# Optimization experiments

Hardware: AMD Instinct MI355X
Metric: run time of the kernel (lower is better)

Reference implementation:

```python
import jax, jax.numpy as jnp
import numpy as np

D = 256          # d_model
NH = 8           # n_heads
HD = D // NH
LEV = 3          # n_levels
NP = 4           # n_points
DFF = 1024       # d_ffn
B = 8            # batch
LQ = 3600        # 60*60 queries (hardcoded in get_reference_points)
SHAPES = np.array([[60, 60], [30, 30], [15, 15]], dtype=np.int64)
LIN = int((SHAPES[:, 0] * SHAPES[:, 1]).sum())  # 4725
START = np.concatenate([[0], np.cumsum(SHAPES[:, 0] * SHAPES[:, 1])[:-1]]).astype(np.int64)


def setup_inputs() -> dict:
    key = jax.random.key(0)
    ks = iter(jax.random.split(key, 32))
    def lin(k, o, i):
        return jax.random.normal(k, (o, i), jnp.float32) * 0.02
    return {
        "tgt": jax.random.normal(next(ks), (LQ, B, D), jnp.float32),
        "query_pos": jax.random.normal(next(ks), (1, 1, D), jnp.float32),
        "src": jax.random.normal(next(ks), (B, LIN, D), jnp.float32),
        "src_spatial_shapes": jnp.asarray(SHAPES),
        "level_start_index": jnp.asarray(START),
        "in_proj_w": lin(next(ks), 3 * D, D),
        "in_proj_b": jnp.zeros((3 * D,), jnp.float32),
        "out_proj_w": lin(next(ks), D, D),
        "out_proj_b": jnp.zeros((D,), jnp.float32),
        "samp_off_w": lin(next(ks), NH * LEV * NP * 2, D),
        "samp_off_b": jax.random.normal(next(ks), (NH * LEV * NP * 2,), jnp.float32) * 0.5,
        "attn_w_w": lin(next(ks), NH * LEV * NP, D),
        "attn_w_b": jnp.zeros((NH * LEV * NP,), jnp.float32),
        "value_proj_w": lin(next(ks), D, D),
        "value_proj_b": jnp.zeros((D,), jnp.float32),
        "cross_out_w": lin(next(ks), D, D),
        "cross_out_b": jnp.zeros((D,), jnp.float32),
        "ln1_g": jnp.ones((D,), jnp.float32), "ln1_b": jnp.zeros((D,), jnp.float32),
        "ln2_g": jnp.ones((D,), jnp.float32), "ln2_b": jnp.zeros((D,), jnp.float32),
        "ln3_g": jnp.ones((D,), jnp.float32), "ln3_b": jnp.zeros((D,), jnp.float32),
        "ffn_w1": lin(next(ks), DFF, D), "ffn_b1": jnp.zeros((DFF,), jnp.float32),
        "ffn_w2": lin(next(ks), D, DFF), "ffn_b2": jnp.zeros((D,), jnp.float32),
    }


def _ln(x, g, b, eps=1e-5):
    m = x.mean(-1, keepdims=True)
    v = ((x - m) ** 2).mean(-1, keepdims=True)
    return (x - m) * jax.lax.rsqrt(v + eps) * g + b


def _self_attn(q_in, k_in, v_in, wqkv, bqkv, wo, bo):
    # torch nn.MultiheadAttention semantics, inputs laid out (seq, batch, embed)
    S, N, _ = q_in.shape
    q = (q_in @ wqkv[:D].T + bqkv[:D]).reshape(S, N, NH, HD)
    k = (k_in @ wqkv[D:2 * D].T + bqkv[D:2 * D]).reshape(S, N, NH, HD)
    v = (v_in @ wqkv[2 * D:].T + bqkv[2 * D:]).reshape(S, N, NH, HD)
    logits = jnp.einsum('snhd,tnhd->nhst', q, k) / np.sqrt(HD).astype(np.float32)
    a = jax.nn.softmax(logits, -1)
    ctx = jnp.einsum('nhst,tnhd->snhd', a, v).reshape(S, N, D)
    return ctx @ wo.T + bo


def _bilinear(v_l, loc, Hl, Wl):
    # v_l: [B, NH, Hl*Wl, HD]; loc: [B, NH, LQ, NP, 2] normalized in [0,1]
    # grid_sample(align_corners=False, padding=zeros): pixel = loc*size - 0.5
    x = loc[..., 0] * Wl - 0.5
    y = loc[..., 1] * Hl - 0.5
    x0 = jnp.floor(x); y0 = jnp.floor(y)
    fx = x - x0; fy = y - y0
    x0 = x0.astype(jnp.int32); y0 = y0.astype(jnp.int32)
    def corner(yi, xi, w):
        valid = ((xi >= 0) & (xi < Wl) & (yi >= 0) & (yi < Hl)).astype(v_l.dtype)
        idx = jnp.clip(yi, 0, Hl - 1) * Wl + jnp.clip(xi, 0, Wl - 1)
        b, h, lq, p = idx.shape
        g = jnp.take_along_axis(v_l, idx.reshape(b, h, lq * p)[..., None], axis=2)
        return g.reshape(b, h, lq, p, HD) * (w * valid)[..., None]
    return (corner(y0, x0, (1 - fx) * (1 - fy))
            + corner(y0, x0 + 1, fx * (1 - fy))
            + corner(y0 + 1, x0, (1 - fx) * fy)
            + corner(y0 + 1, x0 + 1, fx * fy))


def _msdeform(query, ref, src, wso, bso, waw, baw, wv, bv, wo, bo):
    Bq, Lq, _ = query.shape
    value = (src @ wv.T + bv).reshape(Bq, LIN, NH, HD).transpose(0, 2, 1, 3)  # [B,NH,LIN,HD]
    off = (query @ wso.T + bso).reshape(Bq, Lq, NH, LEV, NP, 2)
    aw = (query @ waw.T + baw).reshape(Bq, Lq, NH, LEV * NP)
    aw = jax.nn.softmax(aw, -1).reshape(Bq, Lq, NH, LEV, NP)
    normalizer = jnp.asarray(SHAPES[:, ::-1].copy(), jnp.float32)  # (W, H) per level
    loc = ref[:, :, None, :, None, :] + off / normalizer[None, None, None, :, None, :]
    out = jnp.zeros((Bq, NH, Lq, HD), query.dtype)
    for l in range(LEV):
        Hl, Wl = int(SHAPES[l, 0]), int(SHAPES[l, 1])
        s = int(START[l])
        v_l = value[:, :, s:s + Hl * Wl]
        loc_l = loc[:, :, :, l].transpose(0, 2, 1, 3, 4)      # [B,NH,LQ,NP,2]
        sampled = _bilinear(v_l, loc_l, Hl, Wl)               # [B,NH,LQ,NP,HD]
        out = out + (sampled * aw[:, :, :, l].transpose(0, 2, 1, 3)[..., None]).sum(3)
    out = out.transpose(0, 2, 1, 3).reshape(Bq, Lq, D)
    return out @ wo.T + bo


def _reference_points():
    Hh = Ww = 60
    ys = (jnp.arange(Hh, dtype=jnp.float32) + 0.5) / Hh
    xs = (jnp.arange(Ww, dtype=jnp.float32) + 0.5) / Ww
    yy, xx = jnp.meshgrid(ys, xs, indexing='ij')
    ref = jnp.stack([xx.reshape(-1), yy.reshape(-1)], -1)[None]  # [1, 3600, 2]
    return jnp.broadcast_to(ref[:, :, None, :], (1, Hh * Ww, LEV, 2))


def reference(tgt, query_pos, src, src_spatial_shapes, level_start_index,
              in_proj_w, in_proj_b, out_proj_w, out_proj_b,
              samp_off_w, samp_off_b, attn_w_w, attn_w_b,
              value_proj_w, value_proj_b, cross_out_w, cross_out_b,
              ln1_g, ln1_b, ln2_g, ln2_b, ln3_g, ln3_b,
              ffn_w1, ffn_b1, ffn_w2, ffn_b2):
    # dropout layers are identity (eval mode). spatial shapes are static metadata
    # (SHAPES/START) since slicing sizes must be static under jit.
    q = (tgt + query_pos).transpose(1, 0, 2)
    tgt2 = _self_attn(q, q, tgt.transpose(1, 0, 2), in_proj_w, in_proj_b, out_proj_w, out_proj_b)
    t = _ln(tgt + tgt2.transpose(1, 0, 2), ln2_g, ln2_b)
    ref = _reference_points()
    tq = t.transpose(1, 0, 2)  # permute(1,0,2) -> [B, LQ, D]
    tgt2 = _msdeform(tq + query_pos, ref, src, samp_off_w, samp_off_b,
                     attn_w_w, attn_w_b, value_proj_w, value_proj_b,
                     cross_out_w, cross_out_b)
    tq = _ln(tq + tgt2, ln1_g, ln1_b)
    ff = jax.nn.relu(tq @ ffn_w1.T + ffn_b1) @ ffn_w2.T + ffn_b2
    tq = _ln(tq + ff, ln3_g, ln3_b)
    return tq.transpose(1, 0, 2)  # [LQ, B, D]
```

## Files before the change

kernel.cpp:

```cpp
#include <hip/hip_runtime.h>
#include <hip/hip_bf16.h>
#include <cstddef>
#include <cstdint>

#define D_MODEL 256
#define NHEAD   8
#define HDIM    32
#define NLEV    3
#define NPNT    4
#define DFF     1024
#define BATCH   8
#define LQ      3600
#define LIN     4725
#define MROWS   (BATCH*LQ)

typedef short bf16x8 __attribute__((ext_vector_type(8)));
typedef float f32x4  __attribute__((ext_vector_type(4)));

__device__ __forceinline__ unsigned short f2b(float x) {
    unsigned int u = __float_as_uint(x);
    unsigned int r = (u + 0x7fffu + ((u >> 16) & 1u)) >> 16;
    return (unsigned short)r;
}
__device__ __forceinline__ float b2f(unsigned short s) {
    return __uint_as_float(((unsigned int)s) << 16);
}

#define GLDS16(g, l) __builtin_amdgcn_global_load_lds( \
    (const __attribute__((address_space(1))) void*)(g), \
    (__attribute__((address_space(3))) void*)(l), 16, 0, 0)

#define WTOT 991232
__global__ __launch_bounds__(256) void prep_kernel(
    const float* __restrict__ tgt, unsigned short* __restrict__ tgtb,
    const float* __restrict__ srcf, unsigned short* __restrict__ srcb,
    const float* __restrict__ w_in, const float* __restrict__ w_out,
    const float* __restrict__ w_val, const float* __restrict__ w_cross,
    const float* __restrict__ w_so, const float* __restrict__ w_aw,
    const float* __restrict__ w_f1, const float* __restrict__ w_f2,
    unsigned short* __restrict__ wdst,
    const float* __restrict__ qp, const float* __restrict__ so_b,
    const float* __restrict__ aw_b, float* __restrict__ qpv)
{
    const int bid = blockIdx.x;
    const int tid = threadIdx.x;
    if (bid < 7200) {
        int i = bid * 256 + tid;
        float4 v = ((const float4*)tgt)[i];
        ushort4 o; o.x = f2b(v.x); o.y = f2b(v.y); o.z = f2b(v.z); o.w = f2b(v.w);
        ((ushort4*)tgtb)[i] = o;
    } else if (bid < 16650) {
        int i = (bid - 7200) * 256 + tid;
        float4 v = ((const float4*)srcf)[i];
        ushort4 o; o.x = f2b(v.x); o.y = f2b(v.y); o.z = f2b(v.z); o.w = f2b(v.w);
        ((ushort4*)srcb)[i] = o;
    } else if (bid < 17618) {
        int idx = ((bid - 16650) * 256 + tid) * 4;
        if (idx >= WTOT) return;
        const float* src; int off;
        if      (idx < 196608) { src = w_in;    off = idx; }
        else if (idx < 262144) { src = w_out;   off = idx - 196608; }
        else if (idx < 327680) { src = w_val;   off = idx - 262144; }
        else if (idx < 393216) { src = w_cross; off = idx - 327680; }
        else if (idx < 442368) { src = w_so;    off = idx - 393216; }
        else if (idx < 466944) { src = w_aw;    off = idx - 442368; }
        else if (idx < 729088) { src = w_f1;    off = idx - 466944; }
        else                   { src = w_f2;    off = idx - 729088; }
        float4 v = *(const float4*)(src + off);
        ushort4 o; o.x = f2b(v.x); o.y = f2b(v.y); o.z = f2b(v.z); o.w = f2b(v.w);
        *(ushort4*)(wdst + idx) = o;
    } else {
        int o = (bid - 17618) * 256 + tid;
        if (o >= 768 + 192 + 96) return;
        const float* wrow;
        if (o < 768)       wrow = w_in + (size_t)o * D_MODEL;
        else if (o < 960)  wrow = w_so + (size_t)(o - 768) * D_MODEL;
        else               wrow = w_aw + (size_t)(o - 960) * D_MODEL;
        float acc = 0.f;
        for (int d = 0; d < D_MODEL; ++d) acc += qp[d] * wrow[d];
        qpv[o] = acc;
        if (o >= 768) {
            float bias = (o < 960) ? so_b[o - 768] : aw_b[o - 960];
            qpv[1056 + (o - 768)] = acc + bias;
        }
    }
}

__global__ __launch_bounds__(256) void gemm_bf16(
    const unsigned short* __restrict__ A,
    const unsigned short* __restrict__ W,
    const float* __restrict__ bias,
    const float* __restrict__ bias2, int b2lim,
    float* __restrict__ Cf, unsigned short* __restrict__ Cb,
    int M, int N, int K, int relu)
{
    __shared__ __align__(16) unsigned short As[2 * 128 * 32];
    __shared__ __align__(16) unsigned short Bs[2 * 128 * 32];
    const int tid  = threadIdx.x;
    const int wave = tid >> 6;
    const int lane = tid & 63;
    const int m0 = blockIdx.x * 128;
    const int n0 = blockIdx.y * 128;

    const int lr  = lane >> 2;
    const int lc8 = (lane & 3) * 8;
    int ar0 = m0 + wave * 32 + lr;      if (ar0 > M - 1) ar0 = M - 1;
    int ar1 = m0 + wave * 32 + 16 + lr; if (ar1 > M - 1) ar1 = M - 1;
    int br0 = n0 + wave * 32 + lr;      if (br0 > N - 1) br0 = N - 1;
    int br1 = n0 + wave * 32 + 16 + lr; if (br1 > N - 1) br1 = N - 1;
    const unsigned short* pa0 = A + (size_t)ar0 * K + lc8;
    const unsigned short* pa1 = A + (size_t)ar1 * K + lc8;
    const unsigned short* pb0 = W + (size_t)br0 * K + lc8;
    const unsigned short* pb1 = W + (size_t)br1 * K + lc8;
    unsigned short* la0 = As + wave * 1024;
    unsigned short* la1 = As + wave * 1024 + 512;
    unsigned short* lb0 = Bs + wave * 1024;
    unsigned short* lb1 = Bs + wave * 1024 + 512;

    const int wm = (wave >> 1) * 64;
    const int wn = (wave & 1) * 64;
    const int fr = lane & 15;
    const int fk = (lane >> 4) * 8;

    f32x4 acc[4][4] = {};

    for (int k0 = 0; k0 < K; k0 += 64) {
        GLDS16(pa0, la0); GLDS16(pa0 + 32, la0 + 4096);
        GLDS16(pa1, la1); GLDS16(pa1 + 32, la1 + 4096);
        GLDS16(pb0, lb0); GLDS16(pb0 + 32, lb0 + 4096);
        GLDS16(pb1, lb1); GLDS16(pb1 + 32, lb1 + 4096);
        pa0 += 64; pa1 += 64; pb0 += 64; pb1 += 64;
        __syncthreads();
#pragma unroll
        for (int p = 0; p < 2; ++p) {
            bf16x8 af[4], bfv[4];
#pragma unroll
            for (int i = 0; i < 4; ++i)
                af[i] = *(const bf16x8*)&As[p * 4096 + (wm + i * 16 + fr) * 32 + fk];
#pragma unroll
            for (int j = 0; j < 4; ++j)
                bfv[j] = *(const bf16x8*)&Bs[p * 4096 + (wn + j * 16 + fr) * 32 + fk];
#pragma unroll
            for (int i = 0; i < 4; ++i)
#pragma unroll
                for (int j = 0; j < 4; ++j)
                    acc[i][j] = __builtin_amdgcn_mfma_f32_16x16x32_bf16(
                        af[i], bfv[j], acc[i][j], 0, 0, 0);
        }
        __syncthreads();
    }

    const int quad = lane >> 4;
#pragma unroll
    for (int j = 0; j < 4; ++j) {
        const int col = n0 + wn + j * 16 + fr;
        if (col >= N) continue;
        float bv = 0.f;
        if (bias) bv += bias[col];
        if (bias2 && col < b2lim) bv += bias2[col];
#pragma unroll
        for (int i = 0; i < 4; ++i) {
#pragma unroll
            for (int r = 0; r < 4; ++r) {
                const int row = m0 + wm + i * 16 + quad * 4 + r;
                if (row >= M) continue;
                float v = acc[i][j][r] + bv;
                if (relu) v = fmaxf(v, 0.f);
                if (Cf) Cf[(size_t)row * N + col] = v;
                if (Cb) Cb[(size_t)row * N + col] = f2b(v);
            }
        }
    }
}

__global__ __launch_bounds__(256) void gemm_ln(
    const unsigned short* __restrict__ A,
    const unsigned short* __restrict__ W,
    const float* __restrict__ bias,
    const float* __restrict__ resid,
    const float* __restrict__ g, const float* __restrict__ bb,
    float* __restrict__ outf, unsigned short* __restrict__ outb, int K)
{
    __shared__ __align__(16) unsigned short As[2 * 64 * 32];
    __shared__ __align__(16) unsigned short Bs[2 * 256 * 32];
    const int tid  = threadIdx.x;
    const int wave = tid >> 6;
    const int lane = tid & 63;
    const int m0 = blockIdx.x * 64;

    const int arow = tid >> 2;
    const int akc  = (tid & 3) * 8;
    const unsigned short* pa = A + (size_t)(m0 + arow) * K + akc;
    unsigned short* la = As + tid * 8;
    const unsigned short* pb0 = W + (size_t)(arow)       * K + akc;
    const unsigned short* pb1 = W + (size_t)(64  + arow) * K + akc;
    const unsigned short* pb2 = W + (size_t)(128 + arow) * K + akc;
    const unsigned short* pb3 = W + (size_t)(192 + arow) * K + akc;
    unsigned short* lb0 = Bs + tid * 8;
    unsigned short* lb1 = Bs + 2048 + tid * 8;
    unsigned short* lb2 = Bs + 4096 + tid * 8;
    unsigned short* lb3 = Bs + 6144 + tid * 8;

    const int fr = lane & 15;
    const int fk = (lane >> 4) * 8;
    const int quad = lane >> 4;
    const int colbase = wave * 64;

    f32x4 acc[4][4] = {};

    for (int k0 = 0; k0 < K; k0 += 64) {
        GLDS16(pa, la);        GLDS16(pa + 32, la + 2048);
        GLDS16(pb0, lb0);      GLDS16(pb0 + 32, lb0 + 8192);
        GLDS16(pb1, lb1);      GLDS16(pb1 + 32, lb1 + 8192);
        GLDS16(pb2, lb2);      GLDS16(pb2 + 32, lb2 + 8192);
        GLDS16(pb3, lb3);      GLDS16(pb3 + 32, lb3 + 8192);
        pa += 64; pb0 += 64; pb1 += 64; pb2 += 64; pb3 += 64;
        __syncthreads();
#pragma unroll
        for (int p = 0; p < 2; ++p) {
            bf16x8 af[4], bfv[4];
#pragma unroll
            for (int i = 0; i < 4; ++i)
                af[i] = *(const bf16x8*)&As[p * 2048 + (i * 16 + fr) * 32 + fk];
#pragma unroll
            for (int j = 0; j < 4; ++j)
                bfv[j] = *(const bf16x8*)&Bs[p * 8192 + (colbase + j * 16 + fr) * 32 + fk];
#pragma unroll
            for (int i = 0; i < 4; ++i)
#pragma unroll
                for (int j = 0; j < 4; ++j)
                    acc[i][j] = __builtin_amdgcn_mfma_f32_16x16x32_bf16(
                        af[i], bfv[j], acc[i][j], 0, 0, 0);
        }
        __syncthreads();
    }

    float2* red = (float2*)As;
    float rs[4][4], rq[4][4];
#pragma unroll
    for (int i = 0; i < 4; ++i) {
#pragma unroll
        for (int r = 0; r < 4; ++r) {
            const int row = m0 + i * 16 + quad * 4 + r;
            float s = 0.f, q = 0.f;
#pragma unroll
            for (int j = 0; j < 4; ++j) {
                const int col = colbase + j * 16 + fr;
                float v = acc[i][j][r] + bias[col] + resid[(size_t)row * 256 + col];
                acc[i][j][r] = v;
                s += v; q += v * v;
            }
            rs[i][r] = s; rq[i][r] = q;
        }
    }
#pragma unroll
    for (int off = 1; off < 16; off <<= 1) {
#pragma unroll
        for (int i = 0; i < 4; ++i)
#pragma unroll
            for (int r = 0; r < 4; ++r) {
                rs[i][r] += __shfl_xor(rs[i][r], off);
                rq[i][r] += __shfl_xor(rq[i][r], off);
            }
    }
    if ((lane & 15) == 0) {
#pragma unroll
        for (int i = 0; i < 4; ++i)
#pragma unroll
            for (int r = 0; r < 4; ++r)
                red[wave * 64 + i * 16 + quad * 4 + r] = make_float2(rs[i][r], rq[i][r]);
    }
    __syncthreads();
#pragma unroll
    for (int i = 0; i < 4; ++i) {
#pragma unroll
        for (int r = 0; r < 4; ++r) {
            const int rl = i * 16 + quad * 4 + r;
            const float2 t0 = red[rl], t1 = red[64 + rl], t2 = red[128 + rl], t3 = red[192 + rl];
            const float sum = t0.x + t1.x + t2.x + t3.x;
            const float sq  = t0.y + t1.y + t2.y + t3.y;
            const float mean = sum * (1.f / 256.f);
            const float var  = sq * (1.f / 256.f) - mean * mean;
            const float inv  = rsqrtf(var + 1e-5f);
            const int row = m0 + rl;
#pragma unroll
            for (int j = 0; j < 4; ++j) {
                const int col = colbase + j * 16 + fr;
                const float val = (acc[i][j][r] - mean) * inv * g[col] + bb[col];
                outf[(size_t)row * 256 + col] = val;
                if (outb) outb[(size_t)row * 256 + col] = f2b(val);
            }
        }
    }
}

__global__ __launch_bounds__(256) void cross_ffn_kernel(
    const unsigned short* __restrict__ A,
    const unsigned short* __restrict__ Wcr,
    const float* __restrict__ bcr,
    const float* __restrict__ resid1,
    const float* __restrict__ g1, const float* __restrict__ b1g,
    float* __restrict__ t2,
    const unsigned short* __restrict__ W1,
    const float* __restrict__ b1,
    const unsigned short* __restrict__ W2,
    const float* __restrict__ b2,
    const float* __restrict__ g3, const float* __restrict__ b3g,
    float* __restrict__ outf)
{
    __shared__ __align__(16) unsigned short Wc[16384];
    __shared__ __align__(16) unsigned short hid[2304];
    const int tid  = threadIdx.x;
    const int wave = tid >> 6;
    const int lane = tid & 63;
    const int m0 = blockIdx.x * 32;
    const int fr   = lane & 15;
    const int quad = lane >> 4;
    const int xm   = fr & 7;
    float2* red = (float2*)hid;

#pragma unroll
    for (int j = 0; j < 4; ++j) {
        const int c  = wave * 4 + j;
        const int rA = c * 2 + (lane >> 5);
        const int k8 = (lane & 31) ^ (rA & 7);
        GLDS16(A + (size_t)(m0 + rA) * 256 + k8 * 8, Wc + c * 512);
    }
    int w1off[8], w2off[8];
#pragma unroll
    for (int j = 0; j < 8; ++j) {
        const int c  = wave * 8 + j;
        const int n1 = c * 2 + (lane >> 5);
        const int k1 = (lane & 31) ^ (n1 & 7);
        w1off[j] = n1 * 256 + k1 * 8;
        const int n2 = c * 8 + (lane >> 3);
        const int k2 = (lane & 7) ^ (n2 & 7);
        w2off[j] = n2 * 1024 + k2 * 8;
    }
    __syncthreads();
    bf16x8 af[2][8];
#pragma unroll
    for (int i = 0; i < 2; ++i)
#pragma unroll
        for (int s = 0; s < 8; ++s)
            af[i][s] = *(const bf16x8*)&Wc[((i * 16 + fr) * 32 + ((s * 4 + quad) ^ xm)) * 8];

    f32x4 accc[4][2] = {};
    for (int c = 0; c < 4; ++c) {
        __syncthreads();
#pragma unroll
        for (int j = 0; j < 8; ++j)
            GLDS16(Wcr + (size_t)c * 16384 + w1off[j], Wc + (wave * 8 + j) * 512);
        __syncthreads();
#pragma unroll
        for (int s = 0; s < 8; ++s) {
            bf16x8 bv = *(const bf16x8*)&Wc[((wave * 16 + fr) * 32 + ((s * 4 + quad) ^ xm)) * 8];
            accc[c][0] = __builtin_amdgcn_mfma_f32_16x16x32_bf16(af[0][s], bv, accc[c][0], 0, 0, 0);
            accc[c][1] = __builtin_amdgcn_mfma_f32_16x16x32_bf16(af[1][s], bv, accc[c][1], 0, 0, 0);
        }
    }

    float rs[2][4], rq[2][4];
#pragma unroll
    for (int x = 0; x < 2; ++x) {
#pragma unroll
        for (int r = 0; r < 4; ++r) {
            const int row = m0 + x * 16 + quad * 4 + r;
            float s = 0.f, q = 0.f;
#pragma unroll
            for (int c = 0; c < 4; ++c) {
                const int col = c * 64 + wave * 16 + fr;
                float v = accc[c][x][r] + bcr[col] + resid1[(size_t)row * 256 + col];
                accc[c][x][r] = v;
                s += v; q += v * v;
            }
            rs[x][r] = s; rq[x][r] = q;
        }
    }
#pragma unroll
    for (int off = 1; off < 16; off <<= 1) {
#pragma unroll
        for (int x = 0; x < 2; ++x)
#pragma unroll
            for (int r = 0; r < 4; ++r) {
                rs[x][r] += __shfl_xor(rs[x][r], off);
                rq[x][r] += __shfl_xor(rq[x][r], off);
            }
    }
    if ((lane & 15) == 0) {
#pragma unroll
        for (int x = 0; x < 2; ++x)
#pragma unroll
            for (int r = 0; r < 4; ++r)
                red[wave * 32 + x * 16 + quad * 4 + r] = make_float2(rs[x][r], rq[x][r]);
    }
    __syncthreads();
#pragma unroll
    for (int x = 0; x < 2; ++x) {
#pragma unroll
        for (int r = 0; r < 4; ++r) {
            const int rl = x * 16 + quad * 4 + r;
            const float2 t0 = red[rl], t1 = red[32 + rl], t2r = red[64 + rl], t3 = red[96 + rl];
            const float sum = t0.x + t1.x + t2r.x + t3.x;
            const float sq  = t0.y + t1.y + t2r.y + t3.y;
            const float mean = sum * (1.f / 256.f);
            const float var  = sq * (1.f / 256.f) - mean * mean;
            const float inv  = rsqrtf(var + 1e-5f);
            const int row = m0 + rl;
#pragma unroll
            for (int c = 0; c < 4; ++c) {
                const int col = c * 64 + wave * 16 + fr;
                const float val = (accc[c][x][r] - mean) * inv * g1[col] + b1g[col];
                t2[(size_t)row * 256 + col] = val;
                const int g8 = col >> 3;
                Wc[rl * 256 + ((g8 ^ (rl & 7)) << 3) + (col & 7)] = f2b(val);
            }
        }
    }
    __syncthreads();
#pragma unroll
    for (int i = 0; i < 2; ++i)
#pragma unroll
        for (int s = 0; s < 8; ++s)
            af[i][s] = *(const bf16x8*)&Wc[((i * 16 + fr) * 32 + ((s * 4 + quad) ^ xm)) * 8];

    f32x4 acc2[2][4] = {};

    for (int h = 0; h < 16; ++h) {
        __syncthreads();
#pragma unroll
        for (int j = 0; j < 8; ++j)
            GLDS16(W1 + (size_t)h * 16384 + w1off[j], Wc + (wave * 8 + j) * 512);
        __syncthreads();
        f32x4 acc1[2] = {};
#pragma unroll
        for (int s = 0; s < 8; ++s) {
            bf16x8 bv = *(const bf16x8*)&Wc[((wave * 16 + fr) * 32 + ((s * 4 + quad) ^ xm)) * 8];
            acc1[0] = __builtin_amdgcn_mfma_f32_16x16x32_bf16(af[0][s], bv, acc1[0], 0, 0, 0);
            acc1[1] = __builtin_amdgcn_mfma_f32_16x16x32_bf16(af[1][s], bv, acc1[1], 0, 0, 0);
        }
        const float bias1 = b1[h * 64 + wave * 16 + fr];
#pragma unroll
        for (int i = 0; i < 2; ++i)
#pragma unroll
            for (int r = 0; r < 4; ++r) {
                float v = fmaxf(acc1[i][r] + bias1, 0.f);
                hid[(i * 16 + quad * 4 + r) * 72 + wave * 16 + fr] = f2b(v);
            }
        __syncthreads();
#pragma unroll
        for (int j = 0; j < 8; ++j)
            GLDS16(W2 + (size_t)h * 64 + w2off[j], Wc + (wave * 8 + j) * 512);
        __syncthreads();
#pragma unroll
        for (int s = 0; s < 2; ++s) {
            bf16x8 a2[2], b2v[4];
#pragma unroll
            for (int i = 0; i < 2; ++i)
                a2[i] = *(const bf16x8*)&hid[(i * 16 + fr) * 72 + s * 32 + quad * 8];
#pragma unroll
            for (int j2 = 0; j2 < 4; ++j2) {
                const int nb = wave * 64 + j2 * 16 + fr;
                b2v[j2] = *(const bf16x8*)&Wc[(nb * 8 + ((s * 4 + quad) ^ xm)) * 8];
            }
#pragma unroll
            for (int i = 0; i < 2; ++i)
#pragma unroll
                for (int j2 = 0; j2 < 4; ++j2)
                    acc2[i][j2] = __builtin_amdgcn_mfma_f32_16x16x32_bf16(
                        a2[i], b2v[j2], acc2[i][j2], 0, 0, 0);
        }
    }

    __syncthreads();
    const int colbase = wave * 64;
#pragma unroll
    for (int x = 0; x < 2; ++x) {
#pragma unroll
        for (int r = 0; r < 4; ++r) {
            const int row = m0 + x * 16 + quad * 4 + r;
            float s = 0.f, q = 0.f;
#pragma unroll
            for (int y = 0; y < 4; ++y) {
                const int col = colbase + y * 16 + fr;
                float v = acc2[x][y][r] + b2[col] + t2[(size_t)row * 256 + col];
                acc2[x][y][r] = v;
                s += v; q += v * v;
            }
            rs[x][r] = s; rq[x][r] = q;
        }
    }
#pragma unroll
    for (int off = 1; off < 16; off <<= 1) {
#pragma unroll
        for (int x = 0; x < 2; ++x)
#pragma unroll
            for (int r = 0; r < 4; ++r) {
                rs[x][r] += __shfl_xor(rs[x][r], off);
                rq[x][r] += __shfl_xor(rq[x][r], off);
            }
    }
    if ((lane & 15) == 0) {
#pragma unroll
        for (int x = 0; x < 2; ++x)
#pragma unroll
            for (int r = 0; r < 4; ++r)
                red[wave * 32 + x * 16 + quad * 4 + r] = make_float2(rs[x][r], rq[x][r]);
    }
    __syncthreads();
#pragma unroll
    for (int x = 0; x < 2; ++x) {
#pragma unroll
        for (int r = 0; r < 4; ++r) {
            const int rl = x * 16 + quad * 4 + r;
            const float2 t0 = red[rl], t1 = red[32 + rl], t2r = red[64 + rl], t3 = red[96 + rl];
            const float sum = t0.x + t1.x + t2r.x + t3.x;
            const float sq  = t0.y + t1.y + t2r.y + t3.y;
            const float mean = sum * (1.f / 256.f);
            const float var  = sq * (1.f / 256.f) - mean * mean;
            const float inv  = rsqrtf(var + 1e-5f);
            const int row = m0 + rl;
#pragma unroll
            for (int y = 0; y < 4; ++y) {
                const int col = colbase + y * 16 + fr;
                outf[(size_t)row * 256 + col] = (acc2[x][y][r] - mean) * inv * g3[col] + b3g[col];
            }
        }
    }
}

__global__ __launch_bounds__(256) void self_attn_kernel(
    const unsigned short* __restrict__ qkv, unsigned short* __restrict__ ctx)
{
    __shared__ float sh[8][768];
    __shared__ float ls[8][8][8];
    const int n = blockIdx.x;
    const int t = threadIdx.x;
#pragma unroll
    for (int s = 0; s < 8; ++s) {
        const unsigned short* row = qkv + (size_t)(n * 8 + s) * 768;
        sh[s][t]       = b2f(row[t]);
        sh[s][t + 256] = b2f(row[t + 256]);
        sh[s][t + 512] = b2f(row[t + 512]);
    }
    __syncthreads();
    const int h = t >> 5, j = t & 31;
#pragma unroll
    for (int pair = j; pair < 64; pair += 32) {
        const int s = pair >> 3, tt = pair & 7;
        float acc = 0.f;
#pragma unroll
        for (int d = 0; d < 32; ++d)
            acc += sh[s][h * 32 + d] * sh[tt][256 + h * 32 + d];
        ls[h][s][tt] = acc * 0.17677669529663687f;
    }
    __syncthreads();
    if (t < 64) {
        const int hh = t >> 3, s = t & 7;
        float mx = -1e30f;
        for (int tt = 0; tt < 8; ++tt) mx = fmaxf(mx, ls[hh][s][tt]);
        float sum = 0.f;
        for (int tt = 0; tt < 8; ++tt) { float e = expf(ls[hh][s][tt] - mx); ls[hh][s][tt] = e; sum += e; }
        const float inv = 1.f / sum;
        for (int tt = 0; tt < 8; ++tt) ls[hh][s][tt] *= inv;
    }
    __syncthreads();
#pragma unroll
    for (int s = 0; s < 8; ++s) {
        float acc = 0.f;
#pragma unroll
        for (int tt = 0; tt < 8; ++tt)
            acc += ls[h][s][tt] * sh[tt][512 + h * 32 + j];
        ctx[(size_t)(n * 8 + s) * D_MODEL + h * 32 + j] = f2b(acc);
    }
}

__global__ __launch_bounds__(256) void msdeform_kernel(
    const unsigned short* __restrict__ value,
    const float* __restrict__ comb,
    unsigned short* __restrict__ out)
{
    const int bid = blockIdx.x;
    const int b   = bid & 7;
    const int lq0 = (bid >> 3) * 4;
    const int r    = threadIdx.x >> 6;
    const int lane = threadIdx.x & 63;
    const int h = lane >> 3;
    const int l = lane & 7;
    const int lq = lq0 + r;
    const int m = lq * 8 + b;

    const float* offp = comb + (size_t)m * 288 + h * 24;
    const float* awp  = comb + (size_t)m * 288 + 192 + h * 12;
    float off[24], aw[12];
#pragma unroll
    for (int i = 0; i < 6; ++i) *(float4*)&off[i * 4] = ((const float4*)offp)[i];
#pragma unroll
    for (int i = 0; i < 3; ++i) *(float4*)&aw[i * 4] = ((const float4*)awp)[i];

    float mx = aw[0];
#pragma unroll
    for (int i = 1; i < 12; ++i) mx = fmaxf(mx, aw[i]);
    float se = 0.f;
#pragma unroll
    for (int i = 0; i < 12; ++i) { aw[i] = __expf(aw[i] - mx); se += aw[i]; }
    const float inv = 1.f / se;

    const float refx = ((lq % 60) + 0.5f) * (1.f / 60.f);
    const float refy = ((lq / 60) + 0.5f) * (1.f / 60.f);
    const int HW[3] = {60, 30, 15};
    const int ST[3] = {0, 3600, 4500};

    const unsigned short* vbase = value + (size_t)b * LIN * 256 + h * 32 + l * 4;

    float a0 = 0.f, a1 = 0.f, a2 = 0.f, a3 = 0.f;
#pragma unroll
    for (int lev = 0; lev < NLEV; ++lev) {
        const int Wl = HW[lev], s0 = ST[lev];
        const float fWl = (float)Wl;
#pragma unroll
        for (int p = 0; p < NPNT; ++p) {
            const int pt = lev * 4 + p;
            const float ox = off[lev * 8 + p * 2];
            const float oy = off[lev * 8 + p * 2 + 1];
            const float px = refx * fWl + ox - 0.5f;
            const float py = refy * fWl + oy - 0.5f;
            const float x0f = floorf(px), y0f = floorf(py);
            const float fx = px - x0f, fy = py - y0f;
            const int x0 = (int)x0f, y0 = (int)y0f;
            const float aww = aw[pt] * inv;
            const float vx0 = (x0 >= 0 && x0 < Wl) ? 1.f : 0.f;
            const float vx1 = (x0 >= -1 && x0 < Wl - 1) ? 1.f : 0.f;
            const float vy0 = (y0 >= 0 && y0 < Wl) ? 1.f : 0.f;
            const float vy1 = (y0 >= -1 && y0 < Wl - 1) ? 1.f : 0.f;
            const int xc0 = min(max(x0, 0), Wl - 1);
            const int xc1 = min(max(x0 + 1, 0), Wl - 1);
            const int yc0 = min(max(y0, 0), Wl - 1);
            const int yc1 = min(max(y0 + 1, 0), Wl - 1);
            const int sx  = xc1 - xc0;
            const int syW = (yc1 - yc0) * Wl;
            const int i00 = s0 + yc0 * Wl + xc0;
            const float w00 = (1.f - fx) * (1.f - fy) * aww * vx0 * vy0;
            const float w01 = fx * (1.f - fy) * aww * vx1 * vy0;
            const float w10 = (1.f - fx) * fy * aww * vx0 * vy1;
            const float w11 = fx * fy * aww * vx1 * vy1;
            const int i01 = i00 + sx;
            const int i10 = i00 + syW;
            const int i11 = i10 + sx;
            const ushort4 g00 = *(const ushort4*)(vbase + (size_t)i00 * 256);
            const ushort4 g01 = *(const ushort4*)(vbase + (size_t)i01 * 256);
            const ushort4 g10 = *(const ushort4*)(vbase + (size_t)i10 * 256);
            const ushort4 g11 = *(const ushort4*)(vbase + (size_t)i11 * 256);
            a0 += b2f(g00.x) * w00 + b2f(g01.x) * w01 + b2f(g10.x) * w10 + b2f(g11.x) * w11;
            a1 += b2f(g00.y) * w00 + b2f(g01.y) * w01 + b2f(g10.y) * w10 + b2f(g11.y) * w11;
            a2 += b2f(g00.z) * w00 + b2f(g01.z) * w01 + b2f(g10.z) * w10 + b2f(g11.z) * w11;
            a3 += b2f(g00.w) * w00 + b2f(g01.w) * w01 + b2f(g10.w) * w10 + b2f(g11.w) * w11;
        }
    }
    ushort4 o;
    o.x = f2b(a0); o.y = f2b(a1); o.z = f2b(a2); o.w = f2b(a3);
    *(ushort4*)(out + (size_t)m * 256 + h * 32 + l * 4) = o;
}

extern "C" void kernel_launch(void* const* d_in, const int* in_sizes, int n_in,
                              void* d_out, int out_size, void* d_ws, size_t ws_size,
                              hipStream_t stream)
{
    (void)in_sizes; (void)n_in; (void)out_size; (void)ws_size;
    const float* tgt          = (const float*)d_in[0];
    const float* qp           = (const float*)d_in[1];
    const float* src          = (const float*)d_in[2];
    const float* in_proj_w    = (const float*)d_in[5];
    const float* in_proj_b    = (const float*)d_in[6];
    const float* out_proj_w   = (const float*)d_in[7];
    const float* out_proj_b   = (const float*)d_in[8];
    const float* samp_off_w   = (const float*)d_in[9];
    const float* samp_off_b   = (const float*)d_in[10];
    const float* attn_w_w     = (const float*)d_in[11];
    const float* attn_w_b     = (const float*)d_in[12];
    const float* value_proj_w = (const float*)d_in[13];
    const float* value_proj_b = (const float*)d_in[14];
    const float* cross_out_w  = (const float*)d_in[15];
    const float* cross_out_b  = (const float*)d_in[16];
    const float* ln1_g = (const float*)d_in[17];
    const float* ln1_b = (const float*)d_in[18];
    const float* ln2_g = (const float*)d_in[19];
    const float* ln2_b = (const float*)d_in[20];
    const float* ln3_g = (const float*)d_in[21];
    const float* ln3_b = (const float*)d_in[22];
    const float* ffn_w1 = (const float*)d_in[23];
    const float* ffn_b1 = (const float*)d_in[24];
    const float* ffn_w2 = (const float*)d_in[25];
    const float* ffn_b2 = (const float*)d_in[26];
    float* out = (float*)d_out;

    float* ws    = (float*)d_ws;
    float* t     = ws;
    float* t2    = ws + 7372800;
    float* comb  = ws + 14745600;
    float* qpv   = ws + 23040000;
    float* cbias = qpv + 1056;

    unsigned short* bws    = (unsigned short*)((char*)d_ws + 92165376);
    unsigned short* s1     = bws;
    unsigned short* tgtb   = s1;
    unsigned short* ctxb   = s1;
    unsigned short* tb     = s1;
    unsigned short* s2     = bws + 7372800;
    unsigned short* qkvb   = s2;
    unsigned short* valueb = s2;
    unsigned short* msoutb = s2 + 9676800;
    unsigned short* srcb   = bws + 36864000;
    unsigned short* wtsb   = bws + 46540800;

    prep_kernel<<<17623, 256, 0, stream>>>(tgt, tgtb, src, srcb,
                                           in_proj_w, out_proj_w, value_proj_w,
                                           cross_out_w, samp_off_w, attn_w_w,
                                           ffn_w1, ffn_w2, wtsb,
                                           qp, samp_off_b, attn_w_b, qpv);
    gemm_bf16<<<dim3(225, 6), 256, 0, stream>>>(tgtb, wtsb + 0, in_proj_b, qpv, 512,
                                                nullptr, qkvb, MROWS, 768, 256, 0);
    self_attn_kernel<<<3600, 256, 0, stream>>>(qkvb, ctxb);
    gemm_ln<<<450, 256, 0, stream>>>(ctxb, wtsb + 196608, out_proj_b, tgt,
                                     ln2_g, ln2_b, t, tb, 256);
    gemm_bf16<<<dim3(296, 2), 256, 0, stream>>>(srcb, wtsb + 262144, value_proj_b, nullptr, 0,
                                                nullptr, valueb, BATCH * LIN, 256, 256, 0);
    gemm_bf16<<<dim3(225, 3), 256, 0, stream>>>(tb, wtsb + 393216, cbias, nullptr, 0,
                                                comb, nullptr, MROWS, 288, 256, 0);
    msdeform_kernel<<<7200, 256, 0, stream>>>(valueb, comb, msoutb);
    cross_ffn_kernel<<<900, 256, 0, stream>>>(msoutb, wtsb + 327680, cross_out_b,
                                              t, ln1_g, ln1_b, t2,
                                              wtsb + 466944, ffn_b1,
                                              wtsb + 729088, ffn_b2,
                                              ln3_g, ln3_b, out);
}
```

Baseline: 452.9 us.

## Prefetch next weight tile into LDS while MFMAs consume register copies

In the fused cross-out/LN/FFN kernel, each wave now copies its B-operand slice from LDS into registers, then immediately issues the global_load_lds for the next W1/W2/Wcr chunk into the same buffer. The MFMAs then run while that load is in flight. Because each wave only reads the LDS rows it loaded itself, most __syncthreads barriers are replaced by explicit vmcnt/lgkmcnt waits. This is meant to hide global-load latency and cut barrier stalls. The cost is higher register pressure from holding eight bf16x8 operands, and correctness now depends on the per-wave ownership of buffer regions and on the barrier's implicit wait ordering.

Result: no change. 459.0 us (+1.4%).

```diff
diff --git a/kernel.cpp b/kernel.cpp
--- a/kernel.cpp
+++ b/kernel.cpp
@@ -29,6 +29,9 @@
 #define GLDS16(g, l) __builtin_amdgcn_global_load_lds( \
     (const __attribute__((address_space(1))) void*)(g), \
     (__attribute__((address_space(3))) void*)(l), 16, 0, 0)
+
+#define WAIT_VM0()  asm volatile("s_waitcnt vmcnt(0)" ::: "memory")
+#define WAIT_LGKM0() asm volatile("s_waitcnt lgkmcnt(0)" ::: "memory")
 
 #define WTOT 991232
 __global__ __launch_bounds__(256) void prep_kernel(
@@ -344,19 +347,29 @@
 #pragma unroll
         for (int s = 0; s < 8; ++s)
             af[i][s] = *(const bf16x8*)&Wc[((i * 16 + fr) * 32 + ((s * 4 + quad) ^ xm)) * 8];
-
+    WAIT_LGKM0();
+    __syncthreads();
+
+#pragma unroll
+    for (int j = 0; j < 8; ++j)
+        GLDS16(Wcr + w1off[j], Wc + (wave * 8 + j) * 512);
     f32x4 accc[4][2] = {};
     for (int c = 0; c < 4; ++c) {
-        __syncthreads();
-#pragma unroll
-        for (int j = 0; j < 8; ++j)
-            GLDS16(Wcr + (size_t)c * 16384 + w1off[j], Wc + (wave * 8 + j) * 512);
-        __syncthreads();
+        WAIT_VM0();
+        bf16x8 bv[8];
+#pragma unroll
+        for (int s = 0; s < 8; ++s)
+            bv[s] = *(const bf16x8*)&Wc[((wave * 16 + fr) * 32 + ((s * 4 + quad) ^ xm)) * 8];
+        WAIT_LGKM0();
+        if (c < 3) {
+#pragma unroll
+            for (int j = 0; j < 8; ++j)
+                GLDS16(Wcr + (size_t)(c + 1) * 16384 + w1off[j], Wc + (wave * 8 + j) * 512);
+        }
 #pragma unroll
         for (int s = 0; s < 8; ++s) {
-            bf16x8 bv = *(const bf16x8*)&Wc[((wave * 16 + fr) * 32 + ((s * 4 + quad) ^ xm)) * 8];
-            accc[c][0] = __builtin_amdgcn_mfma_f32_16x16x32_bf16(af[0][s], bv, accc[c][0], 0, 0, 0);
-            accc[c][1] = __builtin_amdgcn_mfma_f32_16x16x32_bf16(af[1][s], bv, accc[c][1], 0, 0, 0);
+            accc[c][0] = __builtin_amdgcn_mfma_f32_16x16x32_bf16(af[0][s], bv[s], accc[c][0], 0, 0, 0);
+            accc[c][1] = __builtin_amdgcn_mfma_f32_16x16x32_bf16(af[1][s], bv[s], accc[c][1], 0, 0, 0);
         }
     }
 
@@ -423,21 +436,30 @@
 #pragma unroll
         for (int s = 0; s < 8; ++s)
             af[i][s] = *(const bf16x8*)&Wc[((i * 16 + fr) * 32 + ((s * 4 + quad) ^ xm)) * 8];
+    WAIT_LGKM0();
+    __syncthreads();
+
+#pragma unroll
+    for (int j = 0; j < 8; ++j)
+        GLDS16(W1 + w1off[j], Wc + (wave * 8 + j) * 512);
+    WAIT_VM0();
 
     f32x4 acc2[2][4] = {};
 
     for (int h = 0; h < 16; ++h) {
-        __syncthreads();
+        bf16x8 bv[8];
+#pragma unroll
+        for (int s = 0; s < 8; ++s)
+            bv[s] = *(const bf16x8*)&Wc[((wave * 16 + fr) * 32 + ((s * 4 + quad) ^ xm)) * 8];
+        WAIT_LGKM0();
 #pragma unroll
         for (int j = 0; j < 8; ++j)
-            GLDS16(W1 + (size_t)h * 16384 + w1off[j], Wc + (wave * 8 + j) * 512);
-        __syncthreads();
+            GLDS16(W2 + (size_t)h * 64 + w2off[j], Wc + (wave * 8 + j) * 512);
         f32x4 acc1[2] = {};
 #pragma unroll
         for (int s = 0; s < 8; ++s) {
-            bf16x8 bv = *(const bf16x8*)&Wc[((wave * 16 + fr) * 32 + ((s * 4 + quad) ^ xm)) * 8];
-            acc1[0] = __builtin_amdgcn_mfma_f32_16x16x32_bf16(af[0][s], bv, acc1[0], 0, 0, 0);
-            acc1[1] = __builtin_amdgcn_mfma_f32_16x16x32_bf16(af[1][s], bv, acc1[1], 0, 0, 0);
+            acc1[0] = __builtin_amdgcn_mfma_f32_16x16x32_bf16(af[0][s], bv[s], acc1[0], 0, 0, 0);
+            acc1[1] = __builtin_amdgcn_mfma_f32_16x16x32_bf16(af[1][s], bv[s], acc1[1], 0, 0, 0);
         }
         const float bias1 = b1[h * 64 + wave * 16 + fr];
 #pragma unroll
@@ -449,15 +471,8 @@
             }
         __syncthreads();
 #pragma unroll
-        for (int j = 0; j < 8; ++j)
-            GLDS16(W2 + (size_t)h * 64 + w2off[j], Wc + (wave * 8 + j) * 512);
-        __syncthreads();
-#pragma unroll
         for (int s = 0; s < 2; ++s) {
             bf16x8 a2[2], b2v[4];
-#pragma unroll
-            for (int i = 0; i < 2; ++i)
-                a2[i] = *(const bf16x8*)&hid[(i * 16 + fr) * 72 + s * 32 + quad * 8];
 #pragma unroll
             for (int j2 = 0; j2 < 4; ++j2) {
                 const int nb = wave * 64 + j2 * 16 + fr;
@@ -465,14 +480,25 @@
             }
 #pragma unroll
             for (int i = 0; i < 2; ++i)
+                a2[i] = *(const bf16x8*)&hid[(i * 16 + fr) * 72 + s * 32 + quad * 8];
+            if (s == 1) {
+                WAIT_LGKM0();
+                if (h < 15) {
+#pragma unroll
+                    for (int j = 0; j < 8; ++j)
+                        GLDS16(W1 + (size_t)(h + 1) * 16384 + w1off[j], Wc + (wave * 8 + j) * 512);
+                }
+            }
+#pragma unroll
+            for (int i = 0; i < 2; ++i)
 #pragma unroll
                 for (int j2 = 0; j2 < 4; ++j2)
                     acc2[i][j2] = __builtin_amdgcn_mfma_f32_16x16x32_bf16(
                         a2[i], b2v[j2], acc2[i][j2], 0, 0, 0);
         }
-    }
-
-    __syncthreads();
+        __syncthreads();
+    }
+
     const int colbase = wave * 64;
 #pragma unroll
     for (int x = 0; x < 2; ++x) {
```
